# Kernel optimization log

Measured on AMD Instinct MI355X. Metric: run time of the kernel, lower is better.

Reference implementation:

```python
import jax, jax.numpy as jnp
import numpy as np
from jax import lax

M = 4096
B = 1024
NSTEPS = 199   # loop runs 200 iters; backward+Adam.step happen on iters 1..199
LR = 0.1
B1, B2, EPS = 0.9, 0.999, 1e-8  # torch.optim.Adam defaults


def setup_inputs() -> dict:
    key = jax.random.key(0)
    k1, k2, k3 = jax.random.split(key, 3)
    mean = jax.random.normal(k1, (M,), dtype=jnp.float32)
    va = jax.random.normal(k2, (M, M), dtype=jnp.float32)
    xt = jax.random.normal(k3, (B, 1, M), dtype=jnp.float32)
    return {"mean": mean, "va": va, "xt": xt}


def reference(mean, va, xt):
    # Loss: f(w) = 0.5*(w-m)^T Q (w-m) + sum_i log(1 + exp(-x_i @ m))
    # The second (logistic) term uses m, not w -> constant gradient-wise.
    # grad_w f = 0.5*(Q + Q^T)(w - m). 199 Adam steps, lr=0.1, w0 = ones.
    m_col = mean[:, None]                      # (M, 1)
    Qs = 0.5 * (va + va.T)                     # symmetrized, precomputed once
    w0 = jnp.ones((M, 1), dtype=mean.dtype)
    zeros = jnp.zeros_like(w0)

    def adam_step(carry, t):
        w, mt, vt = carry
        g = Qs @ (w - m_col)                   # (M, 1) matvec
        mt = B1 * mt + (1.0 - B1) * g
        vt = B2 * vt + (1.0 - B2) * g * g
        bc1 = 1.0 - jnp.power(jnp.float32(B1), t)
        bc2 = 1.0 - jnp.power(jnp.float32(B2), t)
        denom = jnp.sqrt(vt) / jnp.sqrt(bc2) + EPS  # torch Adam formulation
        w = w - (LR / bc1) * mt / denom
        return (w, mt, vt), None

    ts = jnp.arange(1, NSTEPS + 1, dtype=jnp.float32)
    (w, _, _), _ = lax.scan(adam_step, (w0, zeros, zeros), ts)
    return w[:, 0]                             # squeeze -> (M,)
```

## Files before the change

### kernel.cpp

```cpp
#include <hip/hip_runtime.h>
#include <math.h>

#define MDIM   4096
#define NSTEPS 199
#define NBLK   256
#define NTHR   1024
#define B1C    0.9f
#define B2C    0.999f
#define EPSC   1e-8f

typedef unsigned long long u64;

__global__ void prep_qs(const float* __restrict__ va, float* __restrict__ Qs) {
    __shared__ float tile[32][33];
    const int j0 = blockIdx.x * 32;
    const int i0 = blockIdx.y * 32;
    const int tx = threadIdx.x, ty = threadIdx.y;

    for (int k = 0; k < 32; k += 8)
        tile[ty + k][tx] = va[(size_t)(j0 + ty + k) * MDIM + i0 + tx];
    __syncthreads();
    for (int k = 0; k < 32; k += 8) {
        int i = i0 + ty + k;
        float a = va[(size_t)i * MDIM + j0 + tx];
        float b = tile[tx][ty + k];
        Qs[(size_t)i * MDIM + j0 + tx] = 0.5f * (a + b);
    }
}

__global__ void init_state(const float* __restrict__ mean,
                           float* __restrict__ u0,
                           int* __restrict__ flags, int nflags) {
    int i = blockIdx.x * blockDim.x + threadIdx.x;
    if (i < MDIM)   u0[i] = 1.0f - mean[i];
    if (i < nflags) flags[i] = 0;
}

__global__ __launch_bounds__(NTHR) void adam_persist(
        const float* __restrict__ Qs,
        float* u0, float* u1,
        const float* __restrict__ mean,
        float* __restrict__ w_out,
        int* __restrict__ flags, int* __restrict__ go) {
    __shared__ float pr[2][16][17];

    const int tid  = threadIdx.x;
    const int bid  = blockIdx.x;
    const int wave = tid >> 6;
    const int lane = tid & 63;
    const int row  = bid * 16 + wave;
    const int col0 = wave * 256 + lane * 4;

    float4 qreg[16];
#pragma unroll
    for (int r = 0; r < 16; ++r)
        qreg[r] = *(const float4*)(Qs + (size_t)(bid * 16 + r) * MDIM + col0);

    float m = 0.0f, v = 0.0f, b1p = 1.0f, b2p = 1.0f;
    const float mrow = mean[row];
    float ucur = 1.0f - mrow;

    float uv0, uv1, uv2, uv3;
    {
        u64 d0 = __hip_atomic_load((const u64*)(u0 + col0),     __ATOMIC_RELAXED, __HIP_MEMORY_SCOPE_AGENT);
        u64 d1 = __hip_atomic_load((const u64*)(u0 + col0 + 2), __ATOMIC_RELAXED, __HIP_MEMORY_SCOPE_AGENT);
        uv0 = __uint_as_float((unsigned)d0);  uv1 = __uint_as_float((unsigned)(d0 >> 32));
        uv2 = __uint_as_float((unsigned)d1);  uv3 = __uint_as_float((unsigned)(d1 >> 32));
    }

    for (int t = 1; t <= NSTEPS; ++t) {
        float* uout = (t & 1) ? u1 : u0;
        const int b = t & 1;

        float acc[16];
#pragma unroll
        for (int r = 0; r < 16; ++r) {
            float4 q = qreg[r];
            acc[r] = q.x * uv0 + q.y * uv1 + q.z * uv2 + q.w * uv3;
        }

#pragma unroll
        for (int stage = 0; stage < 4; ++stage) {
            const int mask = 32 >> stage;
            const int half = 8 >> stage;
            const bool hi = (lane & mask) != 0;
#pragma unroll
            for (int i = 0; i < half; ++i) {
                float plo = __shfl_xor(acc[i],        mask);
                float phi = __shfl_xor(acc[i + half], mask);
                acc[i] = hi ? (acc[i + half] + phi) : (acc[i] + plo);
            }
        }
        float acc0 = acc[0];
        acc0 += __shfl_xor(acc0, 1);
        acc0 += __shfl_xor(acc0, 2);

        if ((lane & 3) == 0) pr[b][wave][lane >> 2] = acc0;
        __syncthreads();

        float unew = ucur;
        if (lane < 16) {
            float p = pr[b][lane][wave];
            p += __shfl_xor(p, 1);
            p += __shfl_xor(p, 2);
            p += __shfl_xor(p, 4);
            p += __shfl_xor(p, 8);
            const float g = p;

            b1p *= B1C;
            b2p *= B2C;
            m = B1C * m + (1.0f - B1C) * g;
            v = B2C * v + (1.0f - B2C) * g * g;
            const float denom = sqrtf(v) / sqrtf(1.0f - b2p) + EPSC;
            unew = ucur - (0.1f / (1.0f - b1p)) * m / denom;
            ucur = unew;
        }

        if (t < NSTEPS) {
            if (lane == 0)
                __hip_atomic_store(uout + row, unew, __ATOMIC_RELAXED,
                                   __HIP_MEMORY_SCOPE_AGENT);
            __syncthreads();

            if (tid == 0)
                __hip_atomic_store(flags + t * NBLK + bid, 1, __ATOMIC_RELAXED,
                                   __HIP_MEMORY_SCOPE_AGENT);

            if (bid == 0) {
                if (tid < 64) {
                    const u64* f64 = (const u64*)(flags + t * NBLK);
                    const u64 PAIR = 0x0000000100000001ULL;
                    int spin = 0;
                    for (;;) {
                        u64 a = __hip_atomic_load(f64 + lane,      __ATOMIC_RELAXED, __HIP_MEMORY_SCOPE_AGENT);
                        u64 c = __hip_atomic_load(f64 + lane + 64, __ATOMIC_RELAXED, __HIP_MEMORY_SCOPE_AGENT);
                        if (__all((a == PAIR) & (c == PAIR))) break;
                        if (++spin > (1 << 24)) break;
                    }
                    if (tid == 0)
                        __hip_atomic_store(go + t, 1, __ATOMIC_RELAXED,
                                           __HIP_MEMORY_SCOPE_AGENT);
                }
            } else {
                if (tid == 0) {
                    int spin = 0;
                    while (__hip_atomic_load(go + t, __ATOMIC_RELAXED,
                                             __HIP_MEMORY_SCOPE_AGENT) == 0) {
                        if (++spin > (1 << 24)) break;
                    }
                }
            }
            __syncthreads();

            u64 d0 = __hip_atomic_load((const u64*)(uout + col0),     __ATOMIC_RELAXED, __HIP_MEMORY_SCOPE_AGENT);
            u64 d1 = __hip_atomic_load((const u64*)(uout + col0 + 2), __ATOMIC_RELAXED, __HIP_MEMORY_SCOPE_AGENT);
            uv0 = __uint_as_float((unsigned)d0);  uv1 = __uint_as_float((unsigned)(d0 >> 32));
            uv2 = __uint_as_float((unsigned)d1);  uv3 = __uint_as_float((unsigned)(d1 >> 32));
        }
    }

    if (lane == 0) w_out[row] = ucur + mrow;
}

extern "C" void kernel_launch(void* const* d_in, const int* in_sizes, int n_in,
                              void* d_out, int out_size, void* d_ws, size_t ws_size,
                              hipStream_t stream) {
    const float* mean = (const float*)d_in[0];
    const float* va   = (const float*)d_in[1];
    float* w_out = (float*)d_out;

    float* ws = (float*)d_ws;
    float* Qs  = ws;
    float* u0  = ws + (size_t)MDIM * MDIM;
    float* u1  = u0 + MDIM;
    int*   flg = (int*)(u1 + MDIM);
    int*   go  = flg + (NSTEPS + 1) * NBLK;

    const int nflags = (NSTEPS + 1) * NBLK + (NSTEPS + 1);

    prep_qs<<<dim3(MDIM / 32, MDIM / 32), dim3(32, 8), 0, stream>>>(va, Qs);
    init_state<<<(nflags + 255) / 256, 256, 0, stream>>>(mean, u0, flg, nflags);

    void* args[] = { (void*)&Qs, (void*)&u0, (void*)&u1,
                     (void*)&mean, (void*)&w_out, (void*)&flg, (void*)&go };
    hipLaunchCooperativeKernel((const void*)adam_persist,
                               dim3(NBLK), dim3(NTHR), args, 0, stream);
}
```

Measured before the change: 967.6 us.

## Replace flag-gather-plus-go grid barrier with per-step atomic arrival counter

```diff
diff --git a/kernel.cpp b/kernel.cpp
--- a/kernel.cpp
+++ b/kernel.cpp
@@ -30,10 +30,10 @@
 
 __global__ void init_state(const float* __restrict__ mean,
                            float* __restrict__ u0,
-                           int* __restrict__ flags, int nflags) {
+                           int* __restrict__ cnt, int ncnt) {
     int i = blockIdx.x * blockDim.x + threadIdx.x;
-    if (i < MDIM)   u0[i] = 1.0f - mean[i];
-    if (i < nflags) flags[i] = 0;
+    if (i < MDIM) u0[i] = 1.0f - mean[i];
+    if (i < ncnt) cnt[i] = (i == 0) ? NBLK : 0;
 }
 
 __global__ __launch_bounds__(NTHR) void adam_persist(
@@ -41,7 +41,7 @@
         float* u0, float* u1,
         const float* __restrict__ mean,
         float* __restrict__ w_out,
-        int* __restrict__ flags, int* __restrict__ go) {
+        int* __restrict__ cnt) {
     __shared__ float pr[2][16][17];
 
     const int tid  = threadIdx.x;
@@ -60,17 +60,26 @@
     const float mrow = mean[row];
     float ucur = 1.0f - mrow;
 
-    float uv0, uv1, uv2, uv3;
-    {
-        u64 d0 = __hip_atomic_load((const u64*)(u0 + col0),     __ATOMIC_RELAXED, __HIP_MEMORY_SCOPE_AGENT);
-        u64 d1 = __hip_atomic_load((const u64*)(u0 + col0 + 2), __ATOMIC_RELAXED, __HIP_MEMORY_SCOPE_AGENT);
-        uv0 = __uint_as_float((unsigned)d0);  uv1 = __uint_as_float((unsigned)(d0 >> 32));
-        uv2 = __uint_as_float((unsigned)d1);  uv3 = __uint_as_float((unsigned)(d1 >> 32));
-    }
+    for (int t = 1; t <= NSTEPS; ++t) {
+        const float* uin = (t & 1) ? u0 : u1;
+        float*      uout = (t & 1) ? u1 : u0;
+        const int b = t & 1;
 
-    for (int t = 1; t <= NSTEPS; ++t) {
-        float* uout = (t & 1) ? u1 : u0;
-        const int b = t & 1;
+        if (tid == 0) {
+            int spin = 0;
+            while (__hip_atomic_load(cnt + (t - 1), __ATOMIC_RELAXED,
+                                     __HIP_MEMORY_SCOPE_AGENT) != NBLK) {
+                if (++spin > (1 << 24)) break;
+            }
+        }
+        __syncthreads();
+
+        u64 d0 = __hip_atomic_load((const u64*)(uin + col0),     __ATOMIC_RELAXED, __HIP_MEMORY_SCOPE_AGENT);
+        u64 d1 = __hip_atomic_load((const u64*)(uin + col0 + 2), __ATOMIC_RELAXED, __HIP_MEMORY_SCOPE_AGENT);
+        const float uv0 = __uint_as_float((unsigned)d0);
+        const float uv1 = __uint_as_float((unsigned)(d0 >> 32));
+        const float uv2 = __uint_as_float((unsigned)d1);
+        const float uv3 = __uint_as_float((unsigned)(d1 >> 32));
 
         float acc[16];
 #pragma unroll
@@ -123,39 +132,8 @@
             __syncthreads();
 
             if (tid == 0)
-                __hip_atomic_store(flags + t * NBLK + bid, 1, __ATOMIC_RELAXED,
-                                   __HIP_MEMORY_SCOPE_AGENT);
-
-            if (bid == 0) {
-                if (tid < 64) {
-                    const u64* f64 = (const u64*)(flags + t * NBLK);
-                    const u64 PAIR = 0x0000000100000001ULL;
-                    int spin = 0;
-                    for (;;) {
-                        u64 a = __hip_atomic_load(f64 + lane,      __ATOMIC_RELAXED, __HIP_MEMORY_SCOPE_AGENT);
-                        u64 c = __hip_atomic_load(f64 + lane + 64, __ATOMIC_RELAXED, __HIP_MEMORY_SCOPE_AGENT);
-                        if (__all((a == PAIR) & (c == PAIR))) break;
-                        if (++spin > (1 << 24)) break;
-                    }
-                    if (tid == 0)
-                        __hip_atomic_store(go + t, 1, __ATOMIC_RELAXED,
-                                           __HIP_MEMORY_SCOPE_AGENT);
-                }
-            } else {
-                if (tid == 0) {
-                    int spin = 0;
-                    while (__hip_atomic_load(go + t, __ATOMIC_RELAXED,
-                                             __HIP_MEMORY_SCOPE_AGENT) == 0) {
-                        if (++spin > (1 << 24)) break;
-                    }
-                }
-            }
-            __syncthreads();
-
-            u64 d0 = __hip_atomic_load((const u64*)(uout + col0),     __ATOMIC_RELAXED, __HIP_MEMORY_SCOPE_AGENT);
-            u64 d1 = __hip_atomic_load((const u64*)(uout + col0 + 2), __ATOMIC_RELAXED, __HIP_MEMORY_SCOPE_AGENT);
-            uv0 = __uint_as_float((unsigned)d0);  uv1 = __uint_as_float((unsigned)(d0 >> 32));
-            uv2 = __uint_as_float((unsigned)d1);  uv3 = __uint_as_float((unsigned)(d1 >> 32));
+                __hip_atomic_fetch_add(cnt + t, 1, __ATOMIC_RELAXED,
+                                       __HIP_MEMORY_SCOPE_AGENT);
         }
     }
 
@@ -173,16 +151,15 @@
     float* Qs  = ws;
     float* u0  = ws + (size_t)MDIM * MDIM;
     float* u1  = u0 + MDIM;
-    int*   flg = (int*)(u1 + MDIM);
-    int*   go  = flg + (NSTEPS + 1) * NBLK;
+    int*   cnt = (int*)(u1 + MDIM);
 
-    const int nflags = (NSTEPS + 1) * NBLK + (NSTEPS + 1);
+    const int ncnt = NSTEPS + 1;
 
     prep_qs<<<dim3(MDIM / 32, MDIM / 32), dim3(32, 8), 0, stream>>>(va, Qs);
-    init_state<<<(nflags + 255) / 256, 256, 0, stream>>>(mean, u0, flg, nflags);
+    init_state<<<(MDIM + 255) / 256, 256, 0, stream>>>(mean, u0, cnt, ncnt);
 
     void* args[] = { (void*)&Qs, (void*)&u0, (void*)&u1,
-                     (void*)&mean, (void*)&w_out, (void*)&flg, (void*)&go };
+                     (void*)&mean, (void*)&w_out, (void*)&cnt };
     hipLaunchCooperativeKernel((const void*)adam_persist,
                                dim3(NBLK), dim3(NTHR), args, 0, stream);
 }
```

Measured after the change: 1.385 ms. 43.2% more time.

## Replace centralized grid barrier with all-to-all per-block flag broadcast

Applied to the files above, without the earlier changes.

```diff
diff --git a/kernel.cpp b/kernel.cpp
--- a/kernel.cpp
+++ b/kernel.cpp
@@ -30,10 +30,10 @@
 
 __global__ void init_state(const float* __restrict__ mean,
                            float* __restrict__ u0,
-                           int* __restrict__ flags, int nflags) {
+                           int* __restrict__ fpriv, int nf) {
     int i = blockIdx.x * blockDim.x + threadIdx.x;
-    if (i < MDIM)   u0[i] = 1.0f - mean[i];
-    if (i < nflags) flags[i] = 0;
+    if (i < MDIM) u0[i] = 1.0f - mean[i];
+    if (i < nf)   fpriv[i] = 0;
 }
 
 __global__ __launch_bounds__(NTHR) void adam_persist(
@@ -41,7 +41,7 @@
         float* u0, float* u1,
         const float* __restrict__ mean,
         float* __restrict__ w_out,
-        int* __restrict__ flags, int* __restrict__ go) {
+        int* __restrict__ fpriv) {
     __shared__ float pr[2][16][17];
 
     const int tid  = threadIdx.x;
@@ -122,32 +122,21 @@
                                    __HIP_MEMORY_SCOPE_AGENT);
             __syncthreads();
 
-            if (tid == 0)
-                __hip_atomic_store(flags + t * NBLK + bid, 1, __ATOMIC_RELAXED,
-                                   __HIP_MEMORY_SCOPE_AGENT);
+            int* slab = fpriv + (size_t)(t & 1) * NBLK * NBLK;
 
-            if (bid == 0) {
-                if (tid < 64) {
-                    const u64* f64 = (const u64*)(flags + t * NBLK);
-                    const u64 PAIR = 0x0000000100000001ULL;
-                    int spin = 0;
-                    for (;;) {
-                        u64 a = __hip_atomic_load(f64 + lane,      __ATOMIC_RELAXED, __HIP_MEMORY_SCOPE_AGENT);
-                        u64 c = __hip_atomic_load(f64 + lane + 64, __ATOMIC_RELAXED, __HIP_MEMORY_SCOPE_AGENT);
-                        if (__all((a == PAIR) & (c == PAIR))) break;
-                        if (++spin > (1 << 24)) break;
-                    }
-                    if (tid == 0)
-                        __hip_atomic_store(go + t, 1, __ATOMIC_RELAXED,
-                                           __HIP_MEMORY_SCOPE_AGENT);
-                }
-            } else {
-                if (tid == 0) {
-                    int spin = 0;
-                    while (__hip_atomic_load(go + t, __ATOMIC_RELAXED,
-                                             __HIP_MEMORY_SCOPE_AGENT) == 0) {
-                        if (++spin > (1 << 24)) break;
-                    }
+            if (tid < NBLK)
+                __hip_atomic_store(slab + (size_t)tid * NBLK + bid, t,
+                                   __ATOMIC_RELAXED, __HIP_MEMORY_SCOPE_AGENT);
+
+            if (tid < 64) {
+                const u64* f64 = (const u64*)(slab + (size_t)bid * NBLK);
+                const u64 PAIR = ((u64)(unsigned)t << 32) | (unsigned)t;
+                int spin = 0;
+                for (;;) {
+                    u64 a = __hip_atomic_load(f64 + lane,      __ATOMIC_RELAXED, __HIP_MEMORY_SCOPE_AGENT);
+                    u64 c = __hip_atomic_load(f64 + lane + 64, __ATOMIC_RELAXED, __HIP_MEMORY_SCOPE_AGENT);
+                    if (__all((a == PAIR) & (c == PAIR))) break;
+                    if (++spin > (1 << 24)) break;
                 }
             }
             __syncthreads();
@@ -170,19 +159,18 @@
     float* w_out = (float*)d_out;
 
     float* ws = (float*)d_ws;
-    float* Qs  = ws;
-    float* u0  = ws + (size_t)MDIM * MDIM;
-    float* u1  = u0 + MDIM;
-    int*   flg = (int*)(u1 + MDIM);
-    int*   go  = flg + (NSTEPS + 1) * NBLK;
+    float* Qs    = ws;
+    float* u0    = ws + (size_t)MDIM * MDIM;
+    float* u1    = u0 + MDIM;
+    int*   fpriv = (int*)(u1 + MDIM);
 
-    const int nflags = (NSTEPS + 1) * NBLK + (NSTEPS + 1);
+    const int nf = 2 * NBLK * NBLK;
 
     prep_qs<<<dim3(MDIM / 32, MDIM / 32), dim3(32, 8), 0, stream>>>(va, Qs);
-    init_state<<<(nflags + 255) / 256, 256, 0, stream>>>(mean, u0, flg, nflags);
+    init_state<<<(nf + 255) / 256, 256, 0, stream>>>(mean, u0, fpriv, nf);
 
     void* args[] = { (void*)&Qs, (void*)&u0, (void*)&u1,
-                     (void*)&mean, (void*)&w_out, (void*)&flg, (void*)&go };
+                     (void*)&mean, (void*)&w_out, (void*)&fpriv };
     hipLaunchCooperativeKernel((const void*)adam_persist,
                                dim3(NBLK), dim3(NTHR), args, 0, stream);
 }
```

Result: slower. 1.103 ms (+14.0%).
